# Optimization experiments

Hardware: AMD Instinct MI355X
Metric: run time of the kernel (lower is better)

Reference implementation:

```python
import jax, jax.numpy as jnp
import numpy as np

EPS_LN = 1e-10
EPS_NORM = 0.001


def setup_inputs() -> dict:
    key = jax.random.key(0)
    ks = jax.random.split(key, 6)
    B, L, F, P, ZO = 1, 512, 64, 32, 128
    M = jax.random.normal(ks[0], (B, L, F), dtype=jnp.float32)
    M_mask = jnp.ones((B, L), dtype=jnp.float32)
    gamma = jnp.ones((F,), dtype=jnp.float32)
    beta = jnp.zeros((F,), dtype=jnp.float32)
    # glorot-uniform-ish scales
    Wa = jax.random.uniform(ks[1], (P, F), jnp.float32, -0.25, 0.25)
    ba = jnp.zeros((P,), jnp.float32)
    Wb = jax.random.uniform(ks[2], (P, F), jnp.float32, -0.25, 0.25)
    bb = jnp.zeros((P,), jnp.float32)
    # linear_z is zero-init in the original; use small random so output is nontrivial
    Wz = jax.random.uniform(ks[3], (ZO, P * P), jnp.float32, -0.04, 0.04)
    bz = jnp.zeros((ZO,), jnp.float32)
    return {"M": M, "M_mask": M_mask, "gamma": gamma, "beta": beta,
            "Wa": Wa, "ba": ba, "Wb": Wb, "bb": bb, "Wz": Wz, "bz": bz}


def reference(M, M_mask, gamma, beta, Wa, ba, Wb, bb, Wz, bz):
    # LayerNorm over last dim (custom: std = sqrt(var + eps))
    mean = jnp.mean(M, axis=-1, keepdims=True)
    var = jnp.mean((M - mean) ** 2, axis=-1, keepdims=True)
    y = (M - mean) / jnp.sqrt(var + EPS_LN) * gamma + beta  # (B, L, F)
    mask = M_mask[..., None]  # (B, L, 1)
    a = (jnp.einsum('blf,pf->blp', y, Wa) + ba) * mask  # (B, L, P)
    b = (jnp.einsum('blf,pf->blp', y, Wb) + bb) * mask  # (B, L, P)
    B_, L, P = a.shape
    # outer product over pairs (s dim of original einsum is size 1)
    O = jnp.einsum('bid,bje->bijde', a, b).reshape(B_, L, L, P * P)
    Z = jnp.einsum('bijk,zk->bijz', O, Wz) + bz  # (B, L, L, n_feat_out)
    norm = (M_mask[:, :, None] * M_mask[:, None, :])[..., None]  # (B, L, L, 1)
    return Z / (EPS_NORM + norm)
```

## Files before the change

kernel.cpp:

```cpp
#include <hip/hip_runtime.h>
#include <hip/hip_bf16.h>

#define L  512
#define F  64
#define P  32
#define ZO 128
#define JCH 16

constexpr float EPS_LN   = 1e-10f;
constexpr float EPS_NORM = 1e-3f;

typedef short s16x8 __attribute__((ext_vector_type(8)));
typedef float f32x4 __attribute__((ext_vector_type(4)));

__global__ __launch_bounds__(256) void k_ln_proj(
    const float* __restrict__ M, const float* __restrict__ mask,
    const float* __restrict__ gamma, const float* __restrict__ beta,
    const float* __restrict__ Wa, const float* __restrict__ ba,
    const float* __restrict__ Wb, const float* __restrict__ bb,
    float* __restrict__ a, float* __restrict__ b,
    __hip_bfloat16* __restrict__ abf) {
  __shared__ float y_lds[4][F];
  const int wave = threadIdx.x >> 6;
  const int lane = threadIdx.x & 63;
  const int row  = blockIdx.x * 4 + wave;

  float m = M[row * F + lane];
  float s = m;
  #pragma unroll
  for (int o = 32; o >= 1; o >>= 1) s += __shfl_xor(s, o);
  float mean = s * (1.0f / F);
  float d = m - mean;
  float v = d * d;
  #pragma unroll
  for (int o = 32; o >= 1; o >>= 1) v += __shfl_xor(v, o);
  float rstd = rsqrtf(v * (1.0f / F) + EPS_LN);
  float y = d * rstd * gamma[lane] + beta[lane];
  y_lds[wave][lane] = y;
  __syncthreads();

  const float mk = mask[row];
  const float* W    = (lane < P) ? Wa : Wb;
  const float* bias = (lane < P) ? ba : bb;
  const int p = lane & (P - 1);
  float acc = 0.f;
  #pragma unroll 8
  for (int f = 0; f < F; ++f) acc += y_lds[wave][f] * W[p * F + f];
  acc = (acc + bias[p]) * mk;
  if (lane < P) {
    a[row * P + p]   = acc;
    abf[row * P + p] = __float2bfloat16(acc);
  } else {
    b[row * P + p] = acc;
  }
}

__global__ __launch_bounds__(256) void k_T(
    const float* __restrict__ b, const float* __restrict__ Wz,
    __hip_bfloat16* __restrict__ Tbf) {
  const int seg = blockIdx.x * 256 + threadIdx.x;
  const int j0  = blockIdx.y * JCH;

  float4 w[8];
  const float4* wp = (const float4*)(Wz + (size_t)seg * 32);
  #pragma unroll
  for (int q = 0; q < 8; ++q) w[q] = wp[q];

  #pragma unroll 2
  for (int jj = 0; jj < JCH; ++jj) {
    const float* __restrict__ br = b + (size_t)(j0 + jj) * P;
    float acc0 = 0.f, acc1 = 0.f, acc2 = 0.f, acc3 = 0.f;
    #pragma unroll
    for (int q = 0; q < 8; ++q) {
      acc0 += w[q].x * br[q * 4 + 0];
      acc1 += w[q].y * br[q * 4 + 1];
      acc2 += w[q].z * br[q * 4 + 2];
      acc3 += w[q].w * br[q * 4 + 3];
    }
    Tbf[(size_t)(j0 + jj) * (ZO * P) + seg] =
        __float2bfloat16((acc0 + acc1) + (acc2 + acc3));
  }
}

__global__ __launch_bounds__(256, 8) void k_z(
    const __hip_bfloat16* __restrict__ abf,
    const float* __restrict__ mask,
    const __hip_bfloat16* __restrict__ Tbf,
    const float* __restrict__ bz,
    float* __restrict__ Z) {
  const int t     = threadIdx.x;
  const int lane  = t & 63;
  const int w     = t >> 6;
  const int ntile = blockIdx.x * 4 + w;
  const int n0    = ntile * 16;
  const int j     = n0 >> 7;
  const int r16   = lane & 15;
  const int kg    = lane >> 4;

  const s16x8 bfrag =
      *(const s16x8*)((const short*)Tbf + (size_t)(n0 + r16) * P + kg * 8);

  const float mj  = mask[j];
  const float bzv = bz[(n0 & (ZO - 1)) + r16];

  for (int it = 0; it < 16; ++it) {
    const int i0 = blockIdx.y * 256 + it * 16;
    const s16x8 afrag =
        *(const s16x8*)((const short*)abf + (size_t)(i0 + r16) * P + kg * 8);
    f32x4 acc = {0.f, 0.f, 0.f, 0.f};
    acc = __builtin_amdgcn_mfma_f32_16x16x32_bf16(afrag, bfrag, acc, 0, 0, 0);

    float* zb = Z + (size_t)(i0 + kg * 4) * (L * ZO) + (n0 + r16);
    #pragma unroll
    for (int r = 0; r < 4; ++r) {
      const float mi  = mask[i0 + kg * 4 + r];
      const float inv = __builtin_amdgcn_rcpf(EPS_NORM + mi * mj);
      zb[(size_t)r * (L * ZO)] = (acc[r] + bzv) * inv;
    }
  }
}

extern "C" void kernel_launch(void* const* d_in, const int* in_sizes, int n_in,
                              void* d_out, int out_size, void* d_ws, size_t ws_size,
                              hipStream_t stream) {
  const float* M     = (const float*)d_in[0];
  const float* mask  = (const float*)d_in[1];
  const float* gamma = (const float*)d_in[2];
  const float* beta  = (const float*)d_in[3];
  const float* Wa    = (const float*)d_in[4];
  const float* ba    = (const float*)d_in[5];
  const float* Wb    = (const float*)d_in[6];
  const float* bb    = (const float*)d_in[7];
  const float* Wz    = (const float*)d_in[8];
  const float* bz    = (const float*)d_in[9];

  float* Z = (float*)d_out;
  float* a = (float*)d_ws;
  float* b = a + L * P;
  __hip_bfloat16* Tbf = (__hip_bfloat16*)(b + L * P);
  __hip_bfloat16* abf = Tbf + (size_t)L * ZO * P;

  k_ln_proj<<<L / 4, 256, 0, stream>>>(M, mask, gamma, beta, Wa, ba, Wb, bb,
                                       a, b, abf);
  k_T<<<dim3((ZO * P) / 256, L / JCH), 256, 0, stream>>>(b, Wz, Tbf);
  k_z<<<dim3((L * ZO / 16) / 4, 2), 256, 0, stream>>>(abf, mask, Tbf, bz, Z);
}
```

Before: 41.76 us.

## Reorder k_z tiling to fix A fragment and sweep contiguous output columns

Each wave in the final kernel now holds one A fragment and iterates over 16 consecutive N tiles, instead of holding a B fragment and iterating over rows. This makes each wave write a contiguous 256-float span per output row, improving store locality for the large output write. The mask reciprocals and bias values are precomputed once per wave outside the loop. The launch grid is reshaped to match.

```diff
diff --git a/kernel.cpp b/kernel.cpp
--- a/kernel.cpp
+++ b/kernel.cpp
@@ -6,6 +6,7 @@
 #define P  32
 #define ZO 128
 #define JCH 16
+#define LZ (L * ZO)
 
 constexpr float EPS_LN   = 1e-10f;
 constexpr float EPS_NORM = 1e-3f;
@@ -88,34 +89,55 @@
     const __hip_bfloat16* __restrict__ Tbf,
     const float* __restrict__ bz,
     float* __restrict__ Z) {
-  const int t     = threadIdx.x;
-  const int lane  = t & 63;
-  const int w     = t >> 6;
-  const int ntile = blockIdx.x * 4 + w;
-  const int n0    = ntile * 16;
-  const int j     = n0 >> 7;
-  const int r16   = lane & 15;
-  const int kg    = lane >> 4;
+  const int t    = threadIdx.x;
+  const int lane = t & 63;
+  const int w    = t >> 6;
+  const int r16  = lane & 15;
+  const int kg   = lane >> 4;
+  const int i0   = blockIdx.y * 16;
+  const int ng   = blockIdx.x * 4 + w;
+  const int n0   = ng * 256;
 
-  const s16x8 bfrag =
-      *(const s16x8*)((const short*)Tbf + (size_t)(n0 + r16) * P + kg * 8);
+  const s16x8 afrag =
+      *(const s16x8*)((const short*)abf + (size_t)(i0 + r16) * P + kg * 8);
 
-  const float mj  = mask[j];
-  const float bzv = bz[(n0 & (ZO - 1)) + r16];
+  const float4 mi4 = *(const float4*)(mask + i0 + kg * 4);
+  const float mj0 = mask[n0 >> 7];
+  const float mj1 = mask[(n0 >> 7) + 1];
+  float inv0[4], inv1[4];
+  inv0[0] = __builtin_amdgcn_rcpf(EPS_NORM + mi4.x * mj0);
+  inv0[1] = __builtin_amdgcn_rcpf(EPS_NORM + mi4.y * mj0);
+  inv0[2] = __builtin_amdgcn_rcpf(EPS_NORM + mi4.z * mj0);
+  inv0[3] = __builtin_amdgcn_rcpf(EPS_NORM + mi4.w * mj0);
+  inv1[0] = __builtin_amdgcn_rcpf(EPS_NORM + mi4.x * mj1);
+  inv1[1] = __builtin_amdgcn_rcpf(EPS_NORM + mi4.y * mj1);
+  inv1[2] = __builtin_amdgcn_rcpf(EPS_NORM + mi4.z * mj1);
+  inv1[3] = __builtin_amdgcn_rcpf(EPS_NORM + mi4.w * mj1);
 
-  for (int it = 0; it < 16; ++it) {
-    const int i0 = blockIdx.y * 256 + it * 16;
-    const s16x8 afrag =
-        *(const s16x8*)((const short*)abf + (size_t)(i0 + r16) * P + kg * 8);
+  float bzr[8];
+  #pragma unroll
+  for (int k2 = 0; k2 < 8; ++k2) bzr[k2] = bz[k2 * 16 + r16];
+
+  const short* tb = (const short*)Tbf + (size_t)(n0 + r16) * P + kg * 8;
+  float* zb = Z + (size_t)(i0 + kg * 4) * LZ + n0 + r16;
+
+  #pragma unroll
+  for (int q = 0; q < 16; ++q) {
+    const s16x8 bfrag = *(const s16x8*)(tb + (size_t)q * 16 * P);
     f32x4 acc = {0.f, 0.f, 0.f, 0.f};
     acc = __builtin_amdgcn_mfma_f32_16x16x32_bf16(afrag, bfrag, acc, 0, 0, 0);
-
-    float* zb = Z + (size_t)(i0 + kg * 4) * (L * ZO) + (n0 + r16);
-    #pragma unroll
-    for (int r = 0; r < 4; ++r) {
-      const float mi  = mask[i0 + kg * 4 + r];
-      const float inv = __builtin_amdgcn_rcpf(EPS_NORM + mi * mj);
-      zb[(size_t)r * (L * ZO)] = (acc[r] + bzv) * inv;
+    const float bzv = bzr[q & 7];
+    float* zq = zb + q * 16;
+    if (q < 8) {
+      zq[(size_t)0 * LZ] = (acc[0] + bzv) * inv0[0];
+      zq[(size_t)1 * LZ] = (acc[1] + bzv) * inv0[1];
+      zq[(size_t)2 * LZ] = (acc[2] + bzv) * inv0[2];
+      zq[(size_t)3 * LZ] = (acc[3] + bzv) * inv0[3];
+    } else {
+      zq[(size_t)0 * LZ] = (acc[0] + bzv) * inv1[0];
+      zq[(size_t)1 * LZ] = (acc[1] + bzv) * inv1[1];
+      zq[(size_t)2 * LZ] = (acc[2] + bzv) * inv1[2];
+      zq[(size_t)3 * LZ] = (acc[3] + bzv) * inv1[3];
     }
   }
 }
@@ -143,5 +165,5 @@
   k_ln_proj<<<L / 4, 256, 0, stream>>>(M, mask, gamma, beta, Wa, ba, Wb, bb,
                                        a, b, abf);
   k_T<<<dim3((ZO * P) / 256, L / JCH), 256, 0, stream>>>(b, Wz, Tbf);
-  k_z<<<dim3((L * ZO / 16) / 4, 2), 256, 0, stream>>>(abf, mask, Tbf, bz, Z);
+  k_z<<<dim3(64, 32), 256, 0, stream>>>(abf, mask, Tbf, bz, Z);
 }
```

Measured after the change: 41.26 us. About the same (-1.2%).
